# Performance work log

Measured on AMD Instinct MI355X. Metric: run time of the kernel, lower is better.

Reference implementation:

```python
import jax, jax.numpy as jnp
import numpy as np

N_HEADS = 16
HEAD_DIM = 128
ROTARY_DIM = 128  # rotary_pct = 1.0
ROPE_BASE = 10000.0
NEG = -1e9  # stands in for -inf in the additive mask


def _rope_cos_sin(seq_len, dim, base):
    inv_freq = 1.0 / (base ** (jnp.arange(0, dim, 2, dtype=jnp.float32) / dim))
    t = jnp.arange(seq_len, dtype=jnp.float32)
    freqs = jnp.outer(t, inv_freq)               # (S, dim/2)
    emb = jnp.concatenate([freqs, freqs], -1)    # (S, dim)
    return jnp.cos(emb), jnp.sin(emb)


def _rotate_half(x):
    x1, x2 = jnp.split(x, 2, axis=-1)
    return jnp.concatenate([-x2, x1], axis=-1)


def setup_inputs() -> dict:
    key = jax.random.key(0)
    k1, k2, k3 = jax.random.split(key, 3)
    B, S, H = 2, 2048, 2048
    x = jax.random.normal(k1, (B, S, H), dtype=jnp.float32)
    Wqkv = jax.random.normal(k2, (3 * H, H), dtype=jnp.float32) * (H ** -0.5)
    Wout = jax.random.normal(k3, (H, H), dtype=jnp.float32) * (H ** -0.5)
    # causal additive mask: 0 on/below diagonal, large negative above
    causal = jnp.tril(jnp.ones((S, S), dtype=bool))
    attn_mask = jnp.where(causal, 0.0, NEG).astype(jnp.float32)
    attn_mask = jnp.broadcast_to(attn_mask[None, None], (B, 1, S, S))
    return {"x": x, "attn_mask": attn_mask, "Wqkv": Wqkv, "Wout": Wout}


def reference(x, attn_mask, Wqkv, Wout):
    B, S, H = x.shape
    qkv = x @ Wqkv.T                                   # (B,S,3H)
    qkv = qkv.reshape(B, S, 3, N_HEADS, HEAD_DIM)
    qkv = jnp.transpose(qkv, (2, 0, 3, 1, 4))          # (3,B,h,S,d)
    q, k, v = qkv[0], qkv[1], qkv[2]

    cos, sin = _rope_cos_sin(S, ROTARY_DIM, ROPE_BASE)  # (S, rot)
    cos = cos[None, None]                               # (1,1,S,rot)
    sin = sin[None, None]
    q_rot = q[..., :ROTARY_DIM] * cos + _rotate_half(q[..., :ROTARY_DIM]) * sin
    k_rot = k[..., :ROTARY_DIM] * cos + _rotate_half(k[..., :ROTARY_DIM]) * sin
    q = jnp.concatenate([q_rot, q[..., ROTARY_DIM:]], -1)
    k = jnp.concatenate([k_rot, k[..., ROTARY_DIM:]], -1)

    scores = jnp.einsum("bhqd,bhkd->bhqk", q, k) / (HEAD_DIM ** 0.5)
    scores = scores + attn_mask
    weights = jax.nn.softmax(scores, axis=-1)          # dropout=0 (eval)
    attn = jnp.einsum("bhqk,bhkd->bhqd", weights, v)
    attn = jnp.transpose(attn, (0, 2, 1, 3)).reshape(B, S, H)
    return attn @ Wout.T
```

## Files before the change

kernel.cpp:

```cpp
#include <hip/hip_runtime.h>
#include <hip/hip_bf16.h>
#include <stdint.h>

#define S_LEN 2048
#define NH    16
#define HD    128
#define HDIM  2048
#define H3    6144

typedef unsigned short u16;
typedef __attribute__((ext_vector_type(8))) short short8;
typedef __attribute__((ext_vector_type(4))) float floatx4;

__device__ __forceinline__ u16 f2bf(float f) {
  union { float f; uint32_t u; } v; v.f = f;
  uint32_t r = v.u + 0x7fffu + ((v.u >> 16) & 1u);
  return (u16)(r >> 16);
}
__device__ __forceinline__ float bf2f(u16 u) {
  union { uint32_t u; float f; } v; v.u = ((uint32_t)u) << 16;
  return v.f;
}

__device__ __forceinline__ void async16(const void* g, void* l) {
  __builtin_amdgcn_global_load_lds((const __attribute__((address_space(1))) void*)g,
                                   (__attribute__((address_space(3))) void*)l, 16, 0, 0);
}

__global__ void cvt_bf16(const float* __restrict__ src, u16* __restrict__ dst, int n4) {
  int i = blockIdx.x * 256 + threadIdx.x;
  if (i < n4) {
    float4 v = ((const float4*)src)[i];
    ushort4 o;
    o.x = f2bf(v.x); o.y = f2bf(v.y); o.z = f2bf(v.z); o.w = f2bf(v.w);
    ((ushort4*)dst)[i] = o;
  }
}

__global__ void rope_table(float2* __restrict__ cs) {
  int gid = blockIdx.x * 256 + threadIdx.x;
  int s = gid >> 6, i = gid & 63;
  float f = (float)s * exp2f(-(float)i * 0.20762050593046337f);
  float sn, c;
  sincosf(f, &sn, &c);
  cs[gid] = make_float2(c, sn);
}

template <int OUT_F32>
__global__ void gemm_bt(const u16* __restrict__ A, const u16* __restrict__ B,
                        void* __restrict__ Cv, int M, int N, int K) {
  __shared__ __align__(16) u16 As[128 * 32];
  __shared__ __align__(16) u16 Bs[128 * 32];
  const int t = threadIdx.x;
  const int w = t >> 6, lane = t & 63;
  const int wr = w >> 1, wc = w & 1;
  const int row0 = blockIdx.y * 128, col0 = blockIdx.x * 128;
  const int lr = lane & 15, lk = lane >> 4;
  const int srow = lane >> 2, scol = (lane & 3) * 8;

  floatx4 acc[4][4];
#pragma unroll
  for (int i = 0; i < 4; ++i)
#pragma unroll
    for (int j = 0; j < 4; ++j) acc[i][j] = (floatx4){0.f, 0.f, 0.f, 0.f};

  for (int k0 = 0; k0 < K; k0 += 32) {
    __syncthreads();
#pragma unroll
    for (int ss = 0; ss < 2; ++ss) {
      int s = w + ss * 4;
      const u16* gA = A + (size_t)(row0 + s * 16 + srow) * K + k0 + scol;
      const u16* gB = B + (size_t)(col0 + s * 16 + srow) * K + k0 + scol;
      async16(gA, (char*)As + s * 1024);
      async16(gB, (char*)Bs + s * 1024);
    }
    __syncthreads();
    short8 a[4], b[4];
#pragma unroll
    for (int mi = 0; mi < 4; ++mi)
      a[mi] = *(const short8*)((const char*)As + (wr * 64 + mi * 16 + lr) * 64 + lk * 16);
#pragma unroll
    for (int ni = 0; ni < 4; ++ni)
      b[ni] = *(const short8*)((const char*)Bs + (wc * 64 + ni * 16 + lr) * 64 + lk * 16);
#pragma unroll
    for (int mi = 0; mi < 4; ++mi)
#pragma unroll
      for (int ni = 0; ni < 4; ++ni)
        acc[mi][ni] = __builtin_amdgcn_mfma_f32_16x16x32_bf16(a[mi], b[ni], acc[mi][ni], 0, 0, 0);
  }

#pragma unroll
  for (int mi = 0; mi < 4; ++mi)
#pragma unroll
    for (int ni = 0; ni < 4; ++ni)
#pragma unroll
      for (int r = 0; r < 4; ++r) {
        int row = row0 + wr * 64 + mi * 16 + lk * 4 + r;
        int col = col0 + wc * 64 + ni * 16 + lr;
        float v = acc[mi][ni][r];
        if (OUT_F32) ((float*)Cv)[(size_t)row * N + col] = v;
        else         ((u16*)Cv)[(size_t)row * N + col] = f2bf(v);
      }
}

__global__ void rope_qk(const u16* __restrict__ qkvb, const float2* __restrict__ cs,
                        u16* __restrict__ Qt, u16* __restrict__ Kt) {
  const int t = threadIdx.x;
  const int bh = blockIdx.y, s0 = blockIdx.x * 64;
  const int b = bh >> 4, h = bh & 15;
  const int rg = t >> 4;
  const int i4 = (t & 15) * 4;
#pragma unroll
  for (int pass = 0; pass < 4; ++pass) {
    const int s = s0 + pass * 16 + rg;
    float c[4], sn[4];
#pragma unroll
    for (int z = 0; z < 4; ++z) { float2 v = cs[s * 64 + i4 + z]; c[z] = v.x; sn[z] = v.y; }
#pragma unroll
    for (int m = 0; m < 2; ++m) {
      const u16* src = qkvb + (size_t)(b * S_LEN + s) * H3 + m * HDIM + h * HD;
      ushort4 x1 = *(const ushort4*)(src + i4);
      ushort4 x2 = *(const ushort4*)(src + i4 + 64);
      float a1[4] = {bf2f(x1.x), bf2f(x1.y), bf2f(x1.z), bf2f(x1.w)};
      float a2[4] = {bf2f(x2.x), bf2f(x2.y), bf2f(x2.z), bf2f(x2.w)};
      ushort4 o1, o2;
      o1.x = f2bf(a1[0] * c[0] - a2[0] * sn[0]);  o2.x = f2bf(a2[0] * c[0] + a1[0] * sn[0]);
      o1.y = f2bf(a1[1] * c[1] - a2[1] * sn[1]);  o2.y = f2bf(a2[1] * c[1] + a1[1] * sn[1]);
      o1.z = f2bf(a1[2] * c[2] - a2[2] * sn[2]);  o2.z = f2bf(a2[2] * c[2] + a1[2] * sn[2]);
      o1.w = f2bf(a1[3] * c[3] - a2[3] * sn[3]);  o2.w = f2bf(a2[3] * c[3] + a1[3] * sn[3]);
      u16* dst = (m ? Kt : Qt) + (size_t)(bh * S_LEN + s) * HD;
      *(ushort4*)(dst + i4) = o1;
      *(ushort4*)(dst + i4 + 64) = o2;
    }
  }
}

__global__ void v_trans(const u16* __restrict__ qkvb, u16* __restrict__ Vt) {
  __shared__ u16 tile[64][132];
  const int t = threadIdx.x;
  const int bh = blockIdx.y, s0 = blockIdx.x * 64;
  const int b = bh >> 4, h = bh & 15;
#pragma unroll
  for (int it = 0; it < 8; ++it) {
    int u = it * 256 + t;
    int row = u >> 5;
    int d4 = (u & 31) * 4;
    ushort4 vv = *(const ushort4*)(qkvb + (size_t)(b * S_LEN + s0 + row) * H3 + 2 * HDIM + h * HD + d4);
    tile[row][d4 + 0] = vv.x; tile[row][d4 + 1] = vv.y;
    tile[row][d4 + 2] = vv.z; tile[row][d4 + 3] = vv.w;
  }
  __syncthreads();
#pragma unroll
  for (int it = 0; it < 8; ++it) {
    int u = it * 256 + t;
    int d = u >> 4;
    int s4 = (u & 15) * 4;
    ushort4 ov;
    ov.x = tile[s4 + 0][d]; ov.y = tile[s4 + 1][d];
    ov.z = tile[s4 + 2][d]; ov.w = tile[s4 + 3][d];
    *(ushort4*)(Vt + (size_t)(bh * HD + d) * S_LEN + s0 + s4) = ov;
  }
}

__global__ __launch_bounds__(256, 2)
void attn_fwd(const u16* __restrict__ Qt, const u16* __restrict__ Kt,
              const u16* __restrict__ Vt, u16* __restrict__ Ao) {
  __shared__ __align__(16) u16 Ks[32 * 128];
  __shared__ __align__(16) u16 Vs[128 * 32];
  __shared__ __align__(16) u16 P_lds[4][640];
  const int t = threadIdx.x, w = t >> 6, lane = t & 63;
  const int lr = lane & 15, lk = lane >> 4;
  const int lin = blockIdx.x + 16 * blockIdx.y;
  const int xcd = lin & 7, idx = lin >> 3;
  const int bh = xcd * 4 + (idx >> 4);
  const int bx = idx & 15;
  const int b = bh >> 4, h = bh & 15;
  const u16* Qb = Qt + (size_t)bh * S_LEN * HD;
  const u16* Kb = Kt + (size_t)bh * S_LEN * HD;
  const u16* Vb = Vt + (size_t)bh * HD * S_LEN;
  u16* Pw = &P_lds[w][0];
  const float scale = 0.08838834764831845f;

  const int jA = w * 2, jB = w * 2 + 1;
  const int rkA = jA * 4 + (lane >> 4), rkB = jB * 4 + (lane >> 4);
  const int ckA = (((lane & 15) * 16) ^ ((rkA & 7) << 4)) >> 1;
  const int ckB = (((lane & 15) * 16) ^ ((rkB & 7) << 4)) >> 1;
  const int rvA = jA * 16 + (lane >> 2), rvB = jB * 16 + (lane >> 2);
  const int cvA = (((lane & 3) * 16) ^ ((rvA & 3) << 4)) >> 1;
  const int cvB = (((lane & 3) * 16) ^ ((rvB & 3) << 4)) >> 1;

#pragma unroll 1
  for (int half = 0; half < 2; ++half) {
    const int qt = half ? (31 - bx) : bx;
    const int qw0 = qt * 64 + w * 16;
    const int nkt = 2 * qt + 2;

    short8 aq[4];
#pragma unroll
    for (int c = 0; c < 4; ++c)
      aq[c] = *(const short8*)(Qb + (size_t)(qw0 + lr) * HD + c * 32 + lk * 8);

    floatx4 o[8];
#pragma unroll
    for (int i = 0; i < 8; ++i) o[i] = (floatx4){0.f, 0.f, 0.f, 0.f};
    float mrow = -1e30f, lrow = 0.f;

#pragma unroll 1
    for (int kt = 0; kt < nkt; ++kt) {
      const int kv0 = kt * 32;

      __syncthreads();
      async16(Kb + (size_t)(kv0 + rkA) * HD + ckA, (char*)Ks + jA * 1024);
      async16(Kb + (size_t)(kv0 + rkB) * HD + ckB, (char*)Ks + jB * 1024);
      async16(Vb + (size_t)rvA * S_LEN + kv0 + cvA, (char*)Vs + jA * 1024);
      async16(Vb + (size_t)rvB * S_LEN + kv0 + cvB, (char*)Vs + jB * 1024);
      __syncthreads();

      if (kv0 <= qw0 + 15) {
        short8 kc[4];
        floatx4 s0 = (floatx4){0.f,0.f,0.f,0.f}, s1 = (floatx4){0.f,0.f,0.f,0.f};
#pragma unroll
        for (int c = 0; c < 4; ++c)
          kc[c] = *(const short8*)((const char*)Ks + lr * 256 + ((c * 64 + lk * 16) ^ ((lr & 7) << 4)));
        __builtin_amdgcn_s_setprio(1);
#pragma unroll
        for (int c = 0; c < 4; ++c)
          s0 = __builtin_amdgcn_mfma_f32_16x16x32_bf16(kc[c], aq[c], s0, 0, 0, 0);
        __builtin_amdgcn_s_setprio(0);
#pragma unroll
        for (int c = 0; c < 4; ++c)
          kc[c] = *(const short8*)((const char*)Ks + (16 + lr) * 256 + ((c * 64 + lk * 16) ^ ((lr & 7) << 4)));
        __builtin_amdgcn_s_setprio(1);
#pragma unroll
        for (int c = 0; c < 4; ++c)
          s1 = __builtin_amdgcn_mfma_f32_16x16x32_bf16(kc[c], aq[c], s1, 0, 0, 0);
        __builtin_amdgcn_s_setprio(0);

        const bool need_mask = (kv0 + 31) > qw0;
        float p[8];
#pragma unroll
        for (int r = 0; r < 4; ++r) { p[r] = s0[r] * scale; p[4 + r] = s1[r] * scale; }
        if (need_mask) {
          const int q = qw0 + lr;
#pragma unroll
          for (int r = 0; r < 4; ++r) {
            if (kv0 + lk * 4 + r > q)      p[r]     = -1e30f;
            if (kv0 + 16 + lk * 4 + r > q) p[4 + r] = -1e30f;
          }
        }
        float tm = fmaxf(fmaxf(fmaxf(p[0], p[1]), fmaxf(p[2], p[3])),
                         fmaxf(fmaxf(p[4], p[5]), fmaxf(p[6], p[7])));
        tm = fmaxf(tm, __shfl_xor(tm, 16));
        tm = fmaxf(tm, __shfl_xor(tm, 32));

        float e[8];
        if (__all(tm <= mrow + 8.f)) {
#pragma unroll
          for (int i = 0; i < 8; ++i) e[i] = __expf(p[i] - mrow);
        } else {
          float mnew = fmaxf(mrow, tm);
          float alpha = __expf(mrow - mnew);
          mrow = mnew;
#pragma unroll
          for (int i = 0; i < 8; ++i) e[i] = __expf(p[i] - mnew);
          lrow *= alpha;
#pragma unroll
          for (int ni = 0; ni < 8; ++ni)
#pragma unroll
            for (int r = 0; r < 4; ++r) o[ni][r] *= alpha;
        }
        float ps = ((e[0] + e[1]) + (e[2] + e[3])) + ((e[4] + e[5]) + (e[6] + e[7]));
        ps += __shfl_xor(ps, 16);
        ps += __shfl_xor(ps, 32);
        lrow += ps;

        uint32_t d01 = (uint32_t)f2bf(e[0]) | ((uint32_t)f2bf(e[1]) << 16);
        uint32_t d23 = (uint32_t)f2bf(e[2]) | ((uint32_t)f2bf(e[3]) << 16);
        uint32_t d45 = (uint32_t)f2bf(e[4]) | ((uint32_t)f2bf(e[5]) << 16);
        uint32_t d67 = (uint32_t)f2bf(e[6]) | ((uint32_t)f2bf(e[7]) << 16);
        *(uint2*)(Pw + lr * 40 + lk * 4)      = make_uint2(d01, d23);
        *(uint2*)(Pw + lr * 40 + 16 + lk * 4) = make_uint2(d45, d67);
        short8 pa = *(const short8*)(Pw + lr * 40 + lk * 8);

        __builtin_amdgcn_s_setprio(1);
#pragma unroll
        for (int ni = 0; ni < 8; ++ni) {
          short8 vv = *(const short8*)((const char*)Vs + (ni * 16 + lr) * 64 + ((lk * 16) ^ ((lr & 3) << 4)));
          o[ni] = __builtin_amdgcn_mfma_f32_16x16x32_bf16(vv, pa, o[ni], 0, 0, 0);
        }
        __builtin_amdgcn_s_setprio(0);
      }
    }

    float inv = 1.0f / lrow;
    u16* orow = Ao + (size_t)(b * S_LEN + qw0 + lr) * HDIM + h * HD;
#pragma unroll
    for (int ni = 0; ni < 8; ++ni) {
      ushort4 w4;
      w4.x = f2bf(o[ni][0] * inv); w4.y = f2bf(o[ni][1] * inv);
      w4.z = f2bf(o[ni][2] * inv); w4.w = f2bf(o[ni][3] * inv);
      *(ushort4*)(orow + ni * 16 + lk * 4) = w4;
    }
  }
}

extern "C" void kernel_launch(void* const* d_in, const int* in_sizes, int n_in,
                              void* d_out, int out_size, void* d_ws, size_t ws_size,
                              hipStream_t stream) {
  const float* x    = (const float*)d_in[0];
  const float* Wqkv = (const float*)d_in[2];
  const float* Wout = (const float*)d_in[3];
  float* out = (float*)d_out;
  char* ws = (char*)d_ws;

  u16* xb       = (u16*)(ws + 0);
  u16* wqkvb    = (u16*)(ws + 16777216);
  u16* woutb    = (u16*)(ws + 41943040);
  u16* qkvb     = (u16*)(ws + 50331648);
  u16* Qt       = (u16*)(ws + 100663296);
  u16* Kt       = (u16*)(ws + 117440512);
  u16* Vt       = (u16*)(ws + 134217728);
  float2* cs    = (float2*)(ws + 150994944);
  u16* attn_out = xb;

  cvt_bf16<<<8192,  256, 0, stream>>>(x,    xb,    2097152);
  cvt_bf16<<<12288, 256, 0, stream>>>(Wqkv, wqkvb, 3145728);
  cvt_bf16<<<4096,  256, 0, stream>>>(Wout, woutb, 1048576);
  rope_table<<<512, 256, 0, stream>>>(cs);

  gemm_bt<0><<<dim3(48, 32), 256, 0, stream>>>(xb, wqkvb, qkvb, 4096, H3, HDIM);

  rope_qk<<<dim3(32, 32), 256, 0, stream>>>(qkvb, cs, Qt, Kt);
  v_trans<<<dim3(32, 32), 256, 0, stream>>>(qkvb, Vt);

  attn_fwd<<<dim3(16, 32), 256, 0, stream>>>(Qt, Kt, Vt, attn_out);

  gemm_bt<1><<<dim3(16, 32), 256, 0, stream>>>(attn_out, woutb, out, 4096, HDIM, HDIM);
}
```

Baseline: 432.7 us.

## Replace GEMM with 8-wave double-buffered swizzled 128x256 tile kernel

Replaces the simple 128x128, single-buffered GEMM used for the QKV and output projections with an 8-wave kernel. The new kernel uses 128x256 tiles with K steps of 64, double-buffered async LDS loads, an XOR-swizzled LDS layout to avoid bank conflicts, XCD-aware block swizzling, and a phased MFMA schedule raised with s_setprio. The goal is to overlap global loads with MFMA work and to raise data reuse, since the old loop synced twice per 32-wide K step. In exchange it needs 96 KB of dynamic shared memory and many barriers per iteration, and its correctness depends on the hand-placed vmcnt waits.

```diff
diff --git a/kernel.cpp b/kernel.cpp
--- a/kernel.cpp
+++ b/kernel.cpp
@@ -47,16 +47,39 @@
 }
 
 template <int OUT_F32>
-__global__ void gemm_bt(const u16* __restrict__ A, const u16* __restrict__ B,
-                        void* __restrict__ Cv, int M, int N, int K) {
-  __shared__ __align__(16) u16 As[128 * 32];
-  __shared__ __align__(16) u16 Bs[128 * 32];
-  const int t = threadIdx.x;
-  const int w = t >> 6, lane = t & 63;
-  const int wr = w >> 1, wc = w & 1;
-  const int row0 = blockIdx.y * 128, col0 = blockIdx.x * 128;
+__global__ __launch_bounds__(512, 2)
+void gemm8(const u16* __restrict__ A, const u16* __restrict__ B,
+           void* __restrict__ Cv, int K, int N, int ntx) {
+  extern __shared__ char smem[];
+  const int t = threadIdx.x, w = t >> 6, lane = t & 63;
   const int lr = lane & 15, lk = lane >> 4;
-  const int srow = lane >> 2, scol = (lane & 3) * 8;
+  const int wr = w >> 2, wc = w & 3;
+  const int nwg = gridDim.x, cpx = nwg >> 3;
+  const int swz = (blockIdx.x & 7) * cpx + (blockIdx.x >> 3);
+  const int row0 = (swz / ntx) * 128, col0 = (swz % ntx) * 256;
+  const int NT = K >> 6;
+
+  const u16* baseA[2]; const u16* baseB[4];
+#pragma unroll
+  for (int i = 0; i < 2; ++i) {
+    int yy = (w * 2 + i) * 1024 + lane * 16;
+    int r = yy >> 7, c = (yy & 127) ^ ((r & 7) << 4);
+    baseA[i] = A + (size_t)(row0 + r) * K + (c >> 1);
+  }
+#pragma unroll
+  for (int i = 0; i < 4; ++i) {
+    int yy = (w * 4 + i) * 1024 + lane * 16;
+    int r = yy >> 7, c = (yy & 127) ^ ((r & 7) << 4);
+    baseB[i] = B + (size_t)(col0 + r) * K + (c >> 1);
+  }
+  int arow[4], brow[4];
+#pragma unroll
+  for (int i = 0; i < 4; ++i) {
+    arow[i] = (wr * 64 + i * 16 + lr) * 128;
+    brow[i] = (wc * 64 + i * 16 + lr) * 128;
+  }
+  const int cs0 = (lk * 16) ^ ((lr & 7) << 4);
+  const int cs1 = (64 + lk * 16) ^ ((lr & 7) << 4);
 
   floatx4 acc[4][4];
 #pragma unroll
@@ -64,43 +87,108 @@
 #pragma unroll
     for (int j = 0; j < 4; ++j) acc[i][j] = (floatx4){0.f, 0.f, 0.f, 0.f};
 
-  for (int k0 = 0; k0 < K; k0 += 32) {
-    __syncthreads();
-#pragma unroll
-    for (int ss = 0; ss < 2; ++ss) {
-      int s = w + ss * 4;
-      const u16* gA = A + (size_t)(row0 + s * 16 + srow) * K + k0 + scol;
-      const u16* gB = B + (size_t)(col0 + s * 16 + srow) * K + k0 + scol;
-      async16(gA, (char*)As + s * 1024);
-      async16(gB, (char*)Bs + s * 1024);
-    }
-    __syncthreads();
-    short8 a[4], b[4];
-#pragma unroll
-    for (int mi = 0; mi < 4; ++mi)
-      a[mi] = *(const short8*)((const char*)As + (wr * 64 + mi * 16 + lr) * 64 + lk * 16);
-#pragma unroll
-    for (int ni = 0; ni < 4; ++ni)
-      b[ni] = *(const short8*)((const char*)Bs + (wc * 64 + ni * 16 + lr) * 64 + lk * 16);
-#pragma unroll
-    for (int mi = 0; mi < 4; ++mi)
-#pragma unroll
-      for (int ni = 0; ni < 4; ++ni)
-        acc[mi][ni] = __builtin_amdgcn_mfma_f32_16x16x32_bf16(a[mi], b[ni], acc[mi][ni], 0, 0, 0);
-  }
+#define STA(i, kt) async16(baseA[i] + (kt) * 64, smem + (((kt) & 1) << 14) + (w * 2 + (i)) * 1024)
+#define STB(i, kt) async16(baseB[i] + (kt) * 64, smem + 32768 + (((kt) & 1) << 15) + (w * 4 + (i)) * 1024)
+
+  STA(0, 0); STA(1, 0); STB(0, 0); STB(1, 0); STB(2, 0); STB(3, 0);
+
+  short8 am[2][2], b0[2][2], b1[2][2];
+
+#pragma unroll 1
+  for (int kt = 0; kt < NT; ++kt) {
+    const char* pA = smem + ((kt & 1) << 14);
+    const char* pB = smem + 32768 + ((kt & 1) << 15);
+    const bool more = kt + 1 < NT;
+
+    if (more) {
+      STA(0, kt + 1); STA(1, kt + 1);
+      asm volatile("s_waitcnt vmcnt(2)" ::: "memory");
+    } else {
+      asm volatile("s_waitcnt vmcnt(0)" ::: "memory");
+    }
+    __builtin_amdgcn_s_barrier();
+#pragma unroll
+    for (int m2 = 0; m2 < 2; ++m2) {
+      am[m2][0] = *(const short8*)(pA + arow[m2] + cs0);
+      am[m2][1] = *(const short8*)(pA + arow[m2] + cs1);
+    }
+#pragma unroll
+    for (int n2 = 0; n2 < 2; ++n2) {
+      b0[n2][0] = *(const short8*)(pB + brow[n2] + cs0);
+      b0[n2][1] = *(const short8*)(pB + brow[n2] + cs1);
+    }
+    __builtin_amdgcn_s_setprio(1);
+#pragma unroll
+    for (int m2 = 0; m2 < 2; ++m2)
+#pragma unroll
+      for (int n2 = 0; n2 < 2; ++n2) {
+        acc[m2][n2] = __builtin_amdgcn_mfma_f32_16x16x32_bf16(am[m2][0], b0[n2][0], acc[m2][n2], 0, 0, 0);
+        acc[m2][n2] = __builtin_amdgcn_mfma_f32_16x16x32_bf16(am[m2][1], b0[n2][1], acc[m2][n2], 0, 0, 0);
+      }
+    __builtin_amdgcn_s_setprio(0);
+    __builtin_amdgcn_s_barrier();
+
+#pragma unroll
+    for (int n2 = 0; n2 < 2; ++n2) {
+      b1[n2][0] = *(const short8*)(pB + brow[2 + n2] + cs0);
+      b1[n2][1] = *(const short8*)(pB + brow[2 + n2] + cs1);
+    }
+    if (more) { STB(0, kt + 1); STB(1, kt + 1); }
+    __builtin_amdgcn_s_setprio(1);
+#pragma unroll
+    for (int m2 = 0; m2 < 2; ++m2)
+#pragma unroll
+      for (int n2 = 0; n2 < 2; ++n2) {
+        acc[m2][2 + n2] = __builtin_amdgcn_mfma_f32_16x16x32_bf16(am[m2][0], b1[n2][0], acc[m2][2 + n2], 0, 0, 0);
+        acc[m2][2 + n2] = __builtin_amdgcn_mfma_f32_16x16x32_bf16(am[m2][1], b1[n2][1], acc[m2][2 + n2], 0, 0, 0);
+      }
+    __builtin_amdgcn_s_setprio(0);
+    __builtin_amdgcn_s_barrier();
+
+#pragma unroll
+    for (int m2 = 0; m2 < 2; ++m2) {
+      am[m2][0] = *(const short8*)(pA + arow[2 + m2] + cs0);
+      am[m2][1] = *(const short8*)(pA + arow[2 + m2] + cs1);
+    }
+    if (more) { STB(2, kt + 1); STB(3, kt + 1); }
+    __builtin_amdgcn_s_setprio(1);
+#pragma unroll
+    for (int m2 = 0; m2 < 2; ++m2)
+#pragma unroll
+      for (int n2 = 0; n2 < 2; ++n2) {
+        acc[2 + m2][n2] = __builtin_amdgcn_mfma_f32_16x16x32_bf16(am[m2][0], b0[n2][0], acc[2 + m2][n2], 0, 0, 0);
+        acc[2 + m2][n2] = __builtin_amdgcn_mfma_f32_16x16x32_bf16(am[m2][1], b0[n2][1], acc[2 + m2][n2], 0, 0, 0);
+      }
+    __builtin_amdgcn_s_setprio(0);
+    __builtin_amdgcn_s_barrier();
+
+    __builtin_amdgcn_s_setprio(1);
+#pragma unroll
+    for (int m2 = 0; m2 < 2; ++m2)
+#pragma unroll
+      for (int n2 = 0; n2 < 2; ++n2) {
+        acc[2 + m2][2 + n2] = __builtin_amdgcn_mfma_f32_16x16x32_bf16(am[m2][0], b1[n2][0], acc[2 + m2][2 + n2], 0, 0, 0);
+        acc[2 + m2][2 + n2] = __builtin_amdgcn_mfma_f32_16x16x32_bf16(am[m2][1], b1[n2][1], acc[2 + m2][2 + n2], 0, 0, 0);
+      }
+    __builtin_amdgcn_s_setprio(0);
+    __builtin_amdgcn_s_barrier();
+  }
+#undef STA
+#undef STB
 
 #pragma unroll
   for (int mi = 0; mi < 4; ++mi)
 #pragma unroll
-    for (int ni = 0; ni < 4; ++ni)
+    for (int ni = 0; ni < 4; ++ni) {
+      int row = row0 + wr * 64 + mi * 16 + lk * 4;
+      int col = col0 + wc * 64 + ni * 16 + lr;
 #pragma unroll
       for (int r = 0; r < 4; ++r) {
-        int row = row0 + wr * 64 + mi * 16 + lk * 4 + r;
-        int col = col0 + wc * 64 + ni * 16 + lr;
         float v = acc[mi][ni][r];
-        if (OUT_F32) ((float*)Cv)[(size_t)row * N + col] = v;
-        else         ((u16*)Cv)[(size_t)row * N + col] = f2bf(v);
-      }
+        if (OUT_F32) ((float*)Cv)[(size_t)(row + r) * N + col] = v;
+        else         ((u16*)Cv)[(size_t)(row + r) * N + col] = f2bf(v);
+      }
+    }
 }
 
 __global__ void rope_qk(const u16* __restrict__ qkvb, const float2* __restrict__ cs,
@@ -323,17 +411,22 @@
   float2* cs    = (float2*)(ws + 150994944);
   u16* attn_out = xb;
 
+  (void)hipFuncSetAttribute((const void*)gemm8<0>,
+      hipFuncAttributeMaxDynamicSharedMemorySize, 98304);
+  (void)hipFuncSetAttribute((const void*)gemm8<1>,
+      hipFuncAttributeMaxDynamicSharedMemorySize, 98304);
+
   cvt_bf16<<<8192,  256, 0, stream>>>(x,    xb,    2097152);
   cvt_bf16<<<12288, 256, 0, stream>>>(Wqkv, wqkvb, 3145728);
   cvt_bf16<<<4096,  256, 0, stream>>>(Wout, woutb, 1048576);
   rope_table<<<512, 256, 0, stream>>>(cs);
 
-  gemm_bt<0><<<dim3(48, 32), 256, 0, stream>>>(xb, wqkvb, qkvb, 4096, H3, HDIM);
+  gemm8<0><<<768, 512, 98304, stream>>>(xb, wqkvb, qkvb, HDIM, H3, 24);
 
   rope_qk<<<dim3(32, 32), 256, 0, stream>>>(qkvb, cs, Qt, Kt);
   v_trans<<<dim3(32, 32), 256, 0, stream>>>(qkvb, Vt);
 
   attn_fwd<<<dim3(16, 32), 256, 0, stream>>>(Qt, Kt, Vt, attn_out);
 
-  gemm_bt<1><<<dim3(16, 32), 256, 0, stream>>>(attn_out, woutb, out, 4096, HDIM, HDIM);
-}
+  gemm8<1><<<256, 512, 98304, stream>>>(attn_out, woutb, out, HDIM, HDIM, 8);
+}
```

Result: faster. 411.9 us (-4.8%).
